# Kernel tuning notes

Measured on AMD Instinct MI355X. Metric: run time of the kernel, lower is better.

## Reference

```python
import jax, jax.numpy as jnp
import numpy as np

B, T, C = 8, 4096, 192
HIMG, WIMG = 64, 64
NH, HS = 24, 8
MIX_DIM, DECAY_DIM = 32, 64


def _conv2d(x, w, pad):
    # x: [B, C, H, W], w: [Cout, Cin, kh, kw]
    return jax.lax.conv_general_dilated(
        x, w, (1, 1), [(pad, pad), (pad, pad)],
        dimension_numbers=('NCHW', 'OIHW', 'NCHW'))


def setup_inputs() -> dict:
    key = jax.random.key(0)
    ks = jax.random.split(key, 26)
    f = jax.random.normal
    s = 1.0 / np.sqrt(C)
    return {
        'x': f(ks[0], (B, T, C), jnp.float32),
        'maa_x': f(ks[1], (1, 1, C), jnp.float32) * 0.1,
        'maa_w': f(ks[2], (1, 1, C), jnp.float32) * 0.1,
        'maa_k': f(ks[3], (1, 1, C), jnp.float32) * 0.1,
        'maa_v': f(ks[4], (1, 1, C), jnp.float32) * 0.1,
        'maa_r': f(ks[5], (1, 1, C), jnp.float32) * 0.1,
        'maa_g': f(ks[6], (1, 1, C), jnp.float32) * 0.1,
        'maa_w1': f(ks[7], (C, 5 * MIX_DIM), jnp.float32) * 0.01,
        'maa_w2': f(ks[8], (5, MIX_DIM, C), jnp.float32) * 0.01,
        'decay_w1': f(ks[9], (C, DECAY_DIM), jnp.float32) * 0.01,
        'decay_w2': f(ks[10], (DECAY_DIM, C), jnp.float32) * 0.01,
        'spatial_decay': f(ks[11], (1, 1, C), jnp.float32) * 0.5,
        'u': f(ks[12], (NH, HS), jnp.float32) * 0.5,
        'Wr': f(ks[13], (C, C), jnp.float32) * s,
        'Wk': f(ks[14], (C, C), jnp.float32) * s,
        'Wv': f(ks[15], (C, C), jnp.float32) * s,
        'Wg': f(ks[16], (C, C), jnp.float32) * s,
        'Wo': f(ks[17], (C, C), jnp.float32) * s,
        'ln_g': jnp.ones((C,), jnp.float32),
        'ln_b': jnp.zeros((C,), jnp.float32),
        'w_lp': f(ks[18], (C, C), jnp.float32) * s,
        'w_hd': f(ks[19], (C, C, 3), jnp.float32) * s,
        'w_vd': f(ks[20], (C, C, 3), jnp.float32) * s,
        'w_cd': f(ks[21], (C, C, 3, 3), jnp.float32) * (s / 3.0),
        'theta_cd': jnp.full((1,), 0.7, jnp.float32),
    }


def _diff_conv_mix(x2d, w_lp, w_hd, w_vd, w_cd, theta_cd):
    Cc = x2d.shape[1]
    # laplacian-pattern conv from a 1x1 weight (Conv2d_lp)
    k9 = jnp.zeros((Cc, Cc, 9), x2d.dtype)
    k9 = k9.at[:, :, jnp.array([1, 3, 5, 7])].set(w_lp[:, :, None])
    k9 = k9.at[:, :, 4].set(-4.0 * w_lp)
    out = _conv2d(x2d, k9.reshape(Cc, Cc, 3, 3), 1)
    # horizontal difference conv (Conv2d_hd)
    k9 = jnp.zeros((Cc, Cc, 9), x2d.dtype)
    k9 = k9.at[:, :, jnp.array([0, 3, 6])].set(w_hd)
    k9 = k9.at[:, :, jnp.array([2, 5, 8])].set(-w_hd)
    out = out + _conv2d(x2d, k9.reshape(Cc, Cc, 3, 3), 1)
    # vertical difference conv (Conv2d_vd)
    k9 = jnp.zeros((Cc, Cc, 9), x2d.dtype)
    k9 = k9.at[:, :, jnp.array([0, 1, 2])].set(w_vd)
    k9 = k9.at[:, :, jnp.array([6, 7, 8])].set(-w_vd)
    out = out + _conv2d(x2d, k9.reshape(Cc, Cc, 3, 3), 1)
    # central difference conv (Conv2d_cd): normal conv + 1x1 (-theta * kernel sum)
    out = out + _conv2d(x2d, w_cd, 1)
    kd = jnp.sum(w_cd, axis=(2, 3), keepdims=True) * (-theta_cd[0])
    out = out + _conv2d(x2d, kd, 0)
    return out


def reference(x, maa_x, maa_w, maa_k, maa_v, maa_r, maa_g, maa_w1, maa_w2,
              decay_w1, decay_w2, spatial_decay, u, Wr, Wk, Wv, Wg, Wo,
              ln_g, ln_b, w_lp, w_hd, w_vd, w_cd, theta_cd):
    Bb, Tt, Cc = x.shape
    x2d = x.transpose(0, 2, 1).reshape(Bb, Cc, HIMG, WIMG)
    shifted = _diff_conv_mix(x2d, w_lp, w_hd, w_vd, w_cd, theta_cd)
    xx = shifted.reshape(Bb, Cc, Tt).transpose(0, 2, 1) - x  # spatial shift delta

    # data-dependent token mixing (RWKV6 maa)
    xxx = x + xx * maa_x
    tmp = jnp.tanh(xxx @ maa_w1).reshape(Bb, Tt, 5, MIX_DIM)
    m = jnp.einsum('btfd,fdc->fbtc', tmp, maa_w2)  # [5, B, T, C]
    mw, mk, mv, mr, mg = m[0], m[1], m[2], m[3], m[4]
    xw = x + xx * (maa_w + mw)
    xk = x + xx * (maa_k + mk)
    xv = x + xx * (maa_v + mv)
    xr = x + xx * (maa_r + mr)
    xg = x + xx * (maa_g + mg)

    r = xr @ Wr
    k = xk @ Wk
    v = xv @ Wv
    g = jax.nn.silu(xg @ Wg)
    w = spatial_decay + jnp.tanh(xw @ decay_w1) @ decay_w2  # [B, T, C]

    # WKV6 linear recurrence, fp32 state, per-head [HS, HS]
    rh = r.reshape(Bb, Tt, NH, HS).astype(jnp.float32)
    kh = k.reshape(Bb, Tt, NH, HS).astype(jnp.float32)
    vh = v.reshape(Bb, Tt, NH, HS).astype(jnp.float32)
    dh = jnp.exp(-jnp.exp(w.astype(jnp.float32))).reshape(Bb, Tt, NH, HS)
    uf = u.astype(jnp.float32)

    def step(S, inp):  # S: [B, NH, HS(j key), HS(i value)]
        rt, kt, vt, dt = inp  # each [B, NH, HS]
        kv = kt[..., :, None] * vt[..., None, :]
        yt = jnp.einsum('bhj,bhji->bhi', rt, S + uf[None, :, :, None] * kv)
        return dt[..., None] * S + kv, yt

    xs = tuple(a.transpose(1, 0, 2, 3) for a in (rh, kh, vh, dh))  # time-major
    S0 = jnp.zeros((Bb, NH, HS, HS), jnp.float32)
    _, ys = jax.lax.scan(step, S0, xs)
    y = ys.transpose(1, 0, 2, 3).reshape(Bb, Tt, Cc).astype(x.dtype)

    # ln_x then gated output projection
    mu = jnp.mean(y, axis=-1, keepdims=True)
    var = jnp.mean((y - mu) ** 2, axis=-1, keepdims=True)
    yn = (y - mu) * jax.lax.rsqrt(var + 1e-5) * ln_g + ln_b
    return (yn * g) @ Wo
```

## Files before the change

kernel.cpp:

```cpp
#include <hip/hip_runtime.h>
#include <hip/hip_bf16.h>

#define Bq 8
#define Tq 4096
#define Cq 192
#define NHq 24
#define HSq 8
#define Mq (Bq * Tq)

#define CLq 64
#define NCHq (Tq / CLq)
#define TSq 32

typedef short short8 __attribute__((ext_vector_type(8)));
typedef float f32x4 __attribute__((ext_vector_type(4)));

__device__ __forceinline__ unsigned short f2bf(float f) {
    union { float f; unsigned u; } v; v.f = f;
    unsigned u = v.u;
    return (unsigned short)((u + 0x7FFFu + ((u >> 16) & 1u)) >> 16);
}

__global__ void prep_weights_kernel(const float* __restrict__ w_lp,
                                    const float* __restrict__ w_hd,
                                    const float* __restrict__ w_vd,
                                    const float* __restrict__ w_cd,
                                    const float* __restrict__ theta,
                                    unsigned short* __restrict__ Wg) {
    int idx = blockIdx.x * 256 + threadIdx.x;
    if (idx >= Cq * Cq) return;
    int cout = idx / Cq, cin = idx - cout * Cq;
    float t9[9];
#pragma unroll
    for (int t = 0; t < 9; ++t) t9[t] = 0.f;
    float lp = w_lp[idx];
    t9[1] += lp; t9[3] += lp; t9[5] += lp; t9[7] += lp; t9[4] -= 4.f * lp;
    float h0 = w_hd[idx * 3 + 0], h1 = w_hd[idx * 3 + 1], h2 = w_hd[idx * 3 + 2];
    t9[0] += h0; t9[3] += h1; t9[6] += h2;
    t9[2] -= h0; t9[5] -= h1; t9[8] -= h2;
    float v0 = w_vd[idx * 3 + 0], v1 = w_vd[idx * 3 + 1], v2 = w_vd[idx * 3 + 2];
    t9[0] += v0; t9[1] += v1; t9[2] += v2;
    t9[6] -= v0; t9[7] -= v1; t9[8] -= v2;
    float sum = 0.f;
#pragma unroll
    for (int t = 0; t < 9; ++t) {
        float cdv = w_cd[idx * 9 + t];
        t9[t] += cdv; sum += cdv;
    }
    t9[4] -= theta[0] * sum;
#pragma unroll
    for (int t = 0; t < 9; ++t)
        Wg[(size_t)cout * 1728 + t * Cq + cin] = f2bf(t9[t]);
}

__global__ void wtrans_kernel(const float* __restrict__ W,
                              unsigned short* __restrict__ Wt, int K, int N) {
    int idx = blockIdx.x * 256 + threadIdx.x;
    if (idx >= N * K) return;
    int n = idx / K, k = idx - n * K;
    Wt[idx] = f2bf(W[(size_t)k * N + n]);
}

__global__ void w2t_kernel(const float* __restrict__ w2,
                           unsigned short* __restrict__ w2t) {
    int idx = blockIdx.x * 256 + threadIdx.x;
    if (idx >= 5 * 192 * 32) return;
    int f = idx / (192 * 32), rem = idx - f * 192 * 32;
    int n = rem >> 5, k = rem & 31;
    w2t[idx] = f2bf(w2[(size_t)(f * 32 + k) * Cq + n]);
}

__global__ __launch_bounds__(256) void halo_kernel(
    const float* __restrict__ x, unsigned short* __restrict__ xh) {
    int idx = blockIdx.x * 256 + threadIdx.x;
    int c4 = (idx % 48) * 4;
    int cell = idx / 48;
    int hx = cell % 66;
    int rest = cell / 66;
    int hy = rest % 66;
    int bb = rest / 66;
    ushort4 o = make_ushort4(0, 0, 0, 0);
    if (hy >= 1 && hy <= 64 && hx >= 1 && hx <= 64) {
        size_t g = ((size_t)(bb << 12) + (hy - 1) * 64 + (hx - 1)) * Cq + c4;
        float4 v = *(const float4*)&x[g];
        o = make_ushort4(f2bf(v.x), f2bf(v.y), f2bf(v.z), f2bf(v.w));
    }
    *(ushort4*)&xh[(size_t)cell * Cq + c4] = o;
}

__global__ __launch_bounds__(256) void xxx_kernel(
    const float* __restrict__ x, const float* __restrict__ xx,
    const float* __restrict__ maa_x, unsigned short* __restrict__ out) {
    size_t g = ((size_t)blockIdx.x * 256 + threadIdx.x) * 4;
    int c = (int)(g % Cq);
    float4 xv = *(const float4*)&x[g];
    float4 dv = *(const float4*)&xx[g];
    float4 mv = *(const float4*)&maa_x[c];
    ushort4 o = make_ushort4(f2bf(fmaf(dv.x, mv.x, xv.x)), f2bf(fmaf(dv.y, mv.y, xv.y)),
                             f2bf(fmaf(dv.z, mv.z, xv.z)), f2bf(fmaf(dv.w, mv.w, xv.w)));
    *(ushort4*)&out[g] = o;
}

#define GBM 128
#define GBN 64
#define GBK 64

template <int ALOAD, int EPI, int OBF16>
__global__ __launch_bounds__(256) void mgemm_kernel(
    const unsigned short* __restrict__ Asrc,
    const unsigned short* __restrict__ Wt,
    void* __restrict__ Cv, int N, int K,
    const float* __restrict__ aux0) {
    __shared__ unsigned char lds[(GBM + GBN) * GBK * 2];
    unsigned char* Alds = lds;
    unsigned char* Blds = lds + GBM * GBK * 2;
    float* C = (float*)Cv;
    unsigned short* Cb = (unsigned short*)Cv;

    const int tid = threadIdx.x;
    const int wid = tid >> 6, lane = tid & 63;
    const int llo = lane & 15, lhi = lane >> 4;
    const int m0 = blockIdx.x * GBM, n0 = blockIdx.y * GBN;

    f32x4 acc[2][4];
#pragma unroll
    for (int a = 0; a < 2; ++a)
#pragma unroll
        for (int b = 0; b < 4; ++b) {
            f32x4 z = {0.f, 0.f, 0.f, 0.f};
            acc[a][b] = z;
        }

    for (int k0 = 0; k0 < K; k0 += GBK) {
        __syncthreads();
#pragma unroll
        for (int rep = 0; rep < 4; ++rep) {
            int c = tid + rep * 256;
            int row = c >> 3, kseg = c & 7;
            int m = m0 + row;
            short8 val;
            if (ALOAD == 3) {
                val = *(const short8*)&Asrc[(size_t)m * K + k0 + kseg * 8];
            } else {
                int tap = k0 / Cq;
                int cinb = k0 - tap * Cq;
                int t3 = tap / 3;
                int bb = m >> 12, pos = m & 4095;
                int hy = (pos >> 6) + t3;
                int hx = (pos & 63) + tap - t3 * 3;
                size_t g = ((size_t)bb * 4356 + hy * 66 + hx) * Cq + cinb + kseg * 8;
                val = *(const short8*)&Asrc[g];
            }
            *(short8*)(Alds + row * 128 + ((kseg * 16) ^ ((row & 7) << 4))) = val;
        }
#pragma unroll
        for (int rep = 0; rep < 2; ++rep) {
            int c = tid + rep * 256;
            int row = c >> 3, kseg = c & 7;
            int n = n0 + row;
            short8 val = {0, 0, 0, 0, 0, 0, 0, 0};
            if (n < N) val = *(const short8*)&Wt[(size_t)n * K + k0 + kseg * 8];
            *(short8*)(Blds + row * 128 + ((kseg * 16) ^ ((row & 7) << 4))) = val;
        }
        __syncthreads();
#pragma unroll
        for (int kc = 0; kc < 2; ++kc) {
            int kb = kc * 64 + lhi * 16;
            short8 af[2], bq[4];
#pragma unroll
            for (int mf = 0; mf < 2; ++mf) {
                int row = wid * 32 + mf * 16 + llo;
                af[mf] = *(const short8*)(Alds + row * 128 + (kb ^ ((row & 7) << 4)));
            }
#pragma unroll
            for (int nf = 0; nf < 4; ++nf) {
                int row = nf * 16 + llo;
                bq[nf] = *(const short8*)(Blds + row * 128 + (kb ^ ((row & 7) << 4)));
            }
#pragma unroll
            for (int mf = 0; mf < 2; ++mf)
#pragma unroll
                for (int nf = 0; nf < 4; ++nf)
                    acc[mf][nf] = __builtin_amdgcn_mfma_f32_16x16x32_bf16(
                        af[mf], bq[nf], acc[mf][nf], 0, 0, 0);
        }
    }
#pragma unroll
    for (int mf = 0; mf < 2; ++mf) {
#pragma unroll
        for (int nf = 0; nf < 4; ++nf) {
            int n = n0 + nf * 16 + llo;
            if (n >= N) continue;
#pragma unroll
            for (int r = 0; r < 4; ++r) {
                int m = m0 + wid * 32 + mf * 16 + lhi * 4 + r;
                float val = acc[mf][nf][r];
                if (EPI == 1) val -= aux0[(size_t)m * N + n];
                else if (EPI == 2) val = tanhf(val);
                else if (EPI == 3) val = val / (1.f + expf(-val));
                else if (EPI == 4) val = expf(-expf(aux0[n] + val));
                if (OBF16) Cb[(size_t)m * N + n] = f2bf(val);
                else C[(size_t)m * N + n] = val;
            }
        }
    }
}

__global__ __launch_bounds__(256) void mix5_kernel(
    const float* __restrict__ x, const float* __restrict__ xx,
    const unsigned short* __restrict__ tmp_bf,
    const unsigned short* __restrict__ w2t,
    const float* __restrict__ maa_w, const float* __restrict__ maa_k,
    const float* __restrict__ maa_v, const float* __restrict__ maa_r,
    const float* __restrict__ maa_g,
    unsigned short* __restrict__ xw, unsigned short* __restrict__ xr,
    unsigned short* __restrict__ xk, unsigned short* __restrict__ xv,
    unsigned short* __restrict__ xg) {
    const int tid = threadIdx.x;
    const int wid = tid >> 6, lane = tid & 63;
    const int llo = lane & 15, lhi = lane >> 4;
    const int mb = blockIdx.x * 128 + wid * 32;
    const int nb = blockIdx.y * 64;

    short8 aw[5][4];
#pragma unroll
    for (int f = 0; f < 5; ++f)
#pragma unroll
        for (int nf = 0; nf < 4; ++nf)
            aw[f][nf] = *(const short8*)&w2t[((size_t)f * Cq + nb + nf * 16 + llo) * 32 + lhi * 8];

#pragma unroll
    for (int sub = 0; sub < 2; ++sub) {
        short8 bt[5];
        {
            const unsigned short* trow = &tmp_bf[(size_t)(mb + sub * 16 + llo) * 160 + lhi * 8];
#pragma unroll
            for (int f = 0; f < 5; ++f) bt[f] = *(const short8*)&trow[f * 32];
        }
#pragma unroll
        for (int nf = 0; nf < 4; ++nf) {
            f32x4 acc[5];
#pragma unroll
            for (int f = 0; f < 5; ++f) {
                f32x4 z = {0.f, 0.f, 0.f, 0.f};
                acc[f] = __builtin_amdgcn_mfma_f32_16x16x32_bf16(aw[f][nf], bt[f], z, 0, 0, 0);
            }
            int m = mb + sub * 16 + llo;
            int n0 = nb + nf * 16 + lhi * 4;
            size_t g = (size_t)m * Cq + n0;
            float4 xv4 = *(const float4*)&x[g];
            float4 xx4 = *(const float4*)&xx[g];
            float4 mw4 = *(const float4*)&maa_w[n0];
            float4 mk4 = *(const float4*)&maa_k[n0];
            float4 mv4 = *(const float4*)&maa_v[n0];
            float4 mr4 = *(const float4*)&maa_r[n0];
            float4 mg4 = *(const float4*)&maa_g[n0];
            float xvv[4] = {xv4.x, xv4.y, xv4.z, xv4.w};
            float xxv[4] = {xx4.x, xx4.y, xx4.z, xx4.w};
            float mwv[4] = {mw4.x, mw4.y, mw4.z, mw4.w};
            float mkv[4] = {mk4.x, mk4.y, mk4.z, mk4.w};
            float mvv[4] = {mv4.x, mv4.y, mv4.z, mv4.w};
            float mrv[4] = {mr4.x, mr4.y, mr4.z, mr4.w};
            float mgv[4] = {mg4.x, mg4.y, mg4.z, mg4.w};
            ushort4 ow, ok, ov, orr, og;
            unsigned short* owp = (unsigned short*)&ow;
            unsigned short* okp = (unsigned short*)&ok;
            unsigned short* ovp = (unsigned short*)&ov;
            unsigned short* orp = (unsigned short*)&orr;
            unsigned short* ogp = (unsigned short*)&og;
#pragma unroll
            for (int r = 0; r < 4; ++r) {
                owp[r] = f2bf(fmaf(xxv[r], mwv[r] + acc[0][r], xvv[r]));
                okp[r] = f2bf(fmaf(xxv[r], mkv[r] + acc[1][r], xvv[r]));
                ovp[r] = f2bf(fmaf(xxv[r], mvv[r] + acc[2][r], xvv[r]));
                orp[r] = f2bf(fmaf(xxv[r], mrv[r] + acc[3][r], xvv[r]));
                ogp[r] = f2bf(fmaf(xxv[r], mgv[r] + acc[4][r], xvv[r]));
            }
            *(ushort4*)&xw[g] = ow;
            *(ushort4*)&xk[g] = ok;
            *(ushort4*)&xv[g] = ov;
            *(ushort4*)&xr[g] = orr;
            *(ushort4*)&xg[g] = og;
        }
    }
}

__global__ __launch_bounds__(64) void wkv_pass1_kernel(
    const float* __restrict__ k, const float* __restrict__ v,
    const float* __restrict__ d,
    float* __restrict__ Dbuf, float* __restrict__ Cbuf) {
    int chunk = blockIdx.x, hg = blockIdx.y, b = blockIdx.z;
    int lane = threadIdx.x;
    int slot = lane >> 3, i = lane & 7;
    int cbase = hg * 64;
    size_t gbase = ((size_t)b * Tq + (size_t)chunk * CLq) * Cq + cbase;
    __shared__ float ks[TSq][64], vs[TSq][64], ds[TSq][64];
    float S[8], D[8];
#pragma unroll
    for (int j = 0; j < 8; ++j) { S[j] = 0.f; D[j] = 1.f; }
    for (int t0 = 0; t0 < CLq; t0 += TSq) {
        int f = lane & 15, r4 = lane >> 4;
#pragma unroll
        for (int p = 0; p < 8; ++p) {
            int row = r4 + p * 4;
            size_t g = gbase + (size_t)(t0 + row) * Cq + f * 4;
            *(float4*)&ks[row][f * 4] = *(const float4*)&k[g];
            *(float4*)&vs[row][f * 4] = *(const float4*)&v[g];
            *(float4*)&ds[row][f * 4] = *(const float4*)&d[g];
        }
        __syncthreads();
#pragma unroll 8
        for (int t = 0; t < TSq; ++t) {
            float vv = vs[t][lane];
            float4 ka = *(const float4*)&ks[t][slot * 8];
            float4 kb = *(const float4*)&ks[t][slot * 8 + 4];
            float4 da = *(const float4*)&ds[t][slot * 8];
            float4 db = *(const float4*)&ds[t][slot * 8 + 4];
            float kk[8] = {ka.x, ka.y, ka.z, ka.w, kb.x, kb.y, kb.z, kb.w};
            float dd[8] = {da.x, da.y, da.z, da.w, db.x, db.y, db.z, db.w};
#pragma unroll
            for (int j = 0; j < 8; ++j) {
                float kv = kk[j] * vv;
                S[j] = fmaf(dd[j], S[j], kv);
                D[j] *= dd[j];
            }
        }
        __syncthreads();
    }
    size_t dbase = (((size_t)b * NCHq + chunk) * NHq + hg * 8) * 8;
    Dbuf[dbase + lane] = D[i];
    size_t cb = (((size_t)b * NCHq + chunk) * NHq + (hg * 8 + slot)) * 64 + i;
#pragma unroll
    for (int j = 0; j < 8; ++j) Cbuf[cb + j * 8] = S[j];
}

__global__ __launch_bounds__(64) void wkv_pass2_kernel(
    const float* __restrict__ Dbuf, const float* __restrict__ Cbuf,
    float* __restrict__ Sbuf) {
    int bh = blockIdx.x;
    int lane = threadIdx.x;
    int j = lane >> 3, i = lane & 7;
    int b = bh / NHq, h = bh - b * NHq;
    float S = 0.f;
    size_t stride = (size_t)NHq * 64;
    size_t base = ((size_t)b * NCHq * NHq + h) * 64 + j * 8 + i;
    size_t dstride = (size_t)NHq * 8;
    size_t dbase = ((size_t)b * NCHq * NHq + h) * 8 + j;
#pragma unroll 4
    for (int c = 0; c < NCHq; ++c) {
        Sbuf[base + c * stride] = S;
        float D = Dbuf[dbase + c * dstride];
        float C = Cbuf[base + c * stride];
        S = fmaf(D, S, C);
    }
}

__global__ __launch_bounds__(64) void wkv_pass3_kernel(
    const float* __restrict__ r, const float* __restrict__ k,
    const float* __restrict__ v, const float* __restrict__ d,
    const float* __restrict__ u, const float* __restrict__ Sbuf,
    float* __restrict__ y) {
    int chunk = blockIdx.x, hg = blockIdx.y, b = blockIdx.z;
    int lane = threadIdx.x;
    int slot = lane >> 3, i = lane & 7;
    int h = hg * 8 + slot;
    int cbase = hg * 64;
    size_t gbase = ((size_t)b * Tq + (size_t)chunk * CLq) * Cq + cbase;
    __shared__ float rs[TSq][64], ks[TSq][64], vs[TSq][64], ds[TSq][64];
    float S[8], uu[8];
    size_t sb = (((size_t)b * NCHq + chunk) * NHq + h) * 64 + i;
#pragma unroll
    for (int j = 0; j < 8; ++j) {
        S[j] = Sbuf[sb + j * 8];
        uu[j] = u[h * 8 + j];
    }
    for (int t0 = 0; t0 < CLq; t0 += TSq) {
        int f = lane & 15, r4 = lane >> 4;
#pragma unroll
        for (int p = 0; p < 8; ++p) {
            int row = r4 + p * 4;
            size_t g = gbase + (size_t)(t0 + row) * Cq + f * 4;
            *(float4*)&rs[row][f * 4] = *(const float4*)&r[g];
            *(float4*)&ks[row][f * 4] = *(const float4*)&k[g];
            *(float4*)&vs[row][f * 4] = *(const float4*)&v[g];
            *(float4*)&ds[row][f * 4] = *(const float4*)&d[g];
        }
        __syncthreads();
#pragma unroll 8
        for (int t = 0; t < TSq; ++t) {
            float vv = vs[t][lane];
            float4 ra = *(const float4*)&rs[t][slot * 8];
            float4 rb = *(const float4*)&rs[t][slot * 8 + 4];
            float4 ka = *(const float4*)&ks[t][slot * 8];
            float4 kb = *(const float4*)&ks[t][slot * 8 + 4];
            float4 da = *(const float4*)&ds[t][slot * 8];
            float4 db = *(const float4*)&ds[t][slot * 8 + 4];
            float rr[8] = {ra.x, ra.y, ra.z, ra.w, rb.x, rb.y, rb.z, rb.w};
            float kk[8] = {ka.x, ka.y, ka.z, ka.w, kb.x, kb.y, kb.z, kb.w};
            float dd[8] = {da.x, da.y, da.z, da.w, db.x, db.y, db.z, db.w};
            float yv = 0.f;
#pragma unroll
            for (int j = 0; j < 8; ++j) {
                float kv = kk[j] * vv;
                yv = fmaf(rr[j], fmaf(uu[j], kv, S[j]), yv);
                S[j] = fmaf(dd[j], S[j], kv);
            }
            y[gbase + (size_t)(t0 + t) * Cq + lane] = yv;
        }
        __syncthreads();
    }
}

__global__ __launch_bounds__(256) void ln_gate_kernel(
    const float* __restrict__ y, const float* __restrict__ g,
    const float* __restrict__ ln_g, const float* __restrict__ ln_b,
    unsigned short* __restrict__ out) {
    int row = blockIdx.x * 4 + (threadIdx.x >> 6);
    int lane = threadIdx.x & 63;
    const float* yr = y + (size_t)row * Cq;
    float a0 = yr[lane], a1 = yr[lane + 64], a2 = yr[lane + 128];
    float s = a0 + a1 + a2;
    float ss = a0 * a0 + a1 * a1 + a2 * a2;
#pragma unroll
    for (int m = 1; m < 64; m <<= 1) {
        s += __shfl_xor(s, m);
        ss += __shfl_xor(ss, m);
    }
    float mu = s * (1.f / 192.f);
    float var = ss * (1.f / 192.f) - mu * mu;
    float rstd = rsqrtf(var + 1e-5f);
    const float* gr = g + (size_t)row * Cq;
    unsigned short* orow = out + (size_t)row * Cq;
#pragma unroll
    for (int q = 0; q < 3; ++q) {
        int cc = lane + q * 64;
        float yn = (yr[cc] - mu) * rstd * ln_g[cc] + ln_b[cc];
        orow[cc] = f2bf(yn * gr[cc]);
    }
}

extern "C" void kernel_launch(void* const* d_in, const int* in_sizes, int n_in,
                              void* d_out, int out_size, void* d_ws, size_t ws_size,
                              hipStream_t stream) {
    const float* x        = (const float*)d_in[0];
    const float* maa_x    = (const float*)d_in[1];
    const float* maa_w    = (const float*)d_in[2];
    const float* maa_k    = (const float*)d_in[3];
    const float* maa_v    = (const float*)d_in[4];
    const float* maa_r    = (const float*)d_in[5];
    const float* maa_g    = (const float*)d_in[6];
    const float* maa_w1   = (const float*)d_in[7];
    const float* maa_w2   = (const float*)d_in[8];
    const float* decay_w1 = (const float*)d_in[9];
    const float* decay_w2 = (const float*)d_in[10];
    const float* sdecay   = (const float*)d_in[11];
    const float* u        = (const float*)d_in[12];
    const float* Wr       = (const float*)d_in[13];
    const float* Wk       = (const float*)d_in[14];
    const float* Wv       = (const float*)d_in[15];
    const float* Wgp      = (const float*)d_in[16];
    const float* Wo       = (const float*)d_in[17];
    const float* ln_g     = (const float*)d_in[18];
    const float* ln_b     = (const float*)d_in[19];
    const float* w_lp     = (const float*)d_in[20];
    const float* w_hd     = (const float*)d_in[21];
    const float* w_vd     = (const float*)d_in[22];
    const float* w_cd     = (const float*)d_in[23];
    const float* theta    = (const float*)d_in[24];
    float* out = (float*)d_out;

    const size_t BIG = (size_t)Mq * Cq;
    float* ws = (float*)d_ws;
    unsigned short* Wgt_conv = (unsigned short*)ws;
    unsigned short* Wt_maa = Wgt_conv + (size_t)Cq * 1728;
    unsigned short* Wt_r = Wt_maa + 160 * Cq;
    unsigned short* Wt_k = Wt_r + Cq * Cq;
    unsigned short* Wt_v = Wt_k + Cq * Cq;
    unsigned short* Wt_g = Wt_v + Cq * Cq;
    unsigned short* Wt_o = Wt_g + Cq * Cq;
    unsigned short* w2t  = Wt_o + Cq * Cq;
    unsigned short* Wt_d1 = w2t + 5 * 192 * 32;
    unsigned short* Wt_d2 = Wt_d1 + 64 * Cq;
    float* tmp  = ws + 331776;
    float* wtmp = tmp + (size_t)Mq * 160;
    float* buf0 = wtmp + (size_t)Mq * 64;
    float* buf1 = buf0 + BIG;
    float* buf2 = buf1 + BIG;
    float* buf3 = buf2 + BIG;
    float* buf4 = buf3 + BIG;
    float* buf5 = buf4 + BIG;

    unsigned short* tmp_bf = (unsigned short*)tmp;
    float* Dbuf = tmp + (size_t)Mq * 80;
    float* Cbuf = Dbuf + (size_t)Bq * NCHq * NHq * 8;
    float* Sbuf = Cbuf + (size_t)Bq * NCHq * NHq * 64;
    unsigned short* gate_b = (unsigned short*)(Sbuf + (size_t)Bq * NCHq * NHq * 64);

    unsigned short* x_halo = (unsigned short*)buf1;
    unsigned short* xw_b   = (unsigned short*)buf1;
    unsigned short* xxx_b  = (unsigned short*)(buf2 + BIG / 2);
    unsigned short* xv_b   = (unsigned short*)buf2;
    unsigned short* xg_b   = xxx_b;
    unsigned short* xr_b   = (unsigned short*)buf5;
    unsigned short* xk_b   = (unsigned short*)(buf5 + BIG / 2);
    unsigned short* wtmp_b = (unsigned short*)wtmp;

    dim3 blk(256);
    dim3 mg(Mq / GBM, 3);
    dim3 ew(Mq * Cq / 4 / 256);

    prep_weights_kernel<<<dim3(144), blk, 0, stream>>>(w_lp, w_hd, w_vd, w_cd, theta, Wgt_conv);
    wtrans_kernel<<<dim3(120), blk, 0, stream>>>(maa_w1, Wt_maa, Cq, 160);
    wtrans_kernel<<<dim3(144), blk, 0, stream>>>(Wr, Wt_r, Cq, Cq);
    wtrans_kernel<<<dim3(144), blk, 0, stream>>>(Wk, Wt_k, Cq, Cq);
    wtrans_kernel<<<dim3(144), blk, 0, stream>>>(Wv, Wt_v, Cq, Cq);
    wtrans_kernel<<<dim3(144), blk, 0, stream>>>(Wgp, Wt_g, Cq, Cq);
    wtrans_kernel<<<dim3(144), blk, 0, stream>>>(Wo, Wt_o, Cq, Cq);
    w2t_kernel<<<dim3(120), blk, 0, stream>>>(maa_w2, w2t);
    wtrans_kernel<<<dim3(48), blk, 0, stream>>>(decay_w1, Wt_d1, Cq, 64);
    wtrans_kernel<<<dim3(48), blk, 0, stream>>>(decay_w2, Wt_d2, 64, Cq);
    halo_kernel<<<dim3(8 * 66 * 66 * 48 / 256), blk, 0, stream>>>(x, x_halo);
    mgemm_kernel<1, 1, 0><<<mg, blk, 0, stream>>>(x_halo, Wgt_conv, buf0, Cq, 1728, x);
    xxx_kernel<<<ew, blk, 0, stream>>>(x, buf0, maa_x, xxx_b);
    mgemm_kernel<3, 2, 1><<<mg, blk, 0, stream>>>(xxx_b, Wt_maa, tmp_bf, 160, Cq, nullptr);
    mix5_kernel<<<dim3(Mq / 128, 3), blk, 0, stream>>>(
        x, buf0, tmp_bf, w2t, maa_w, maa_k, maa_v, maa_r, maa_g,
        xw_b, xr_b, xk_b, xv_b, xg_b);
    mgemm_kernel<3, 0, 0><<<mg, blk, 0, stream>>>(xv_b, Wt_v, buf3, Cq, Cq, nullptr);
    mgemm_kernel<3, 3, 0><<<mg, blk, 0, stream>>>(xg_b, Wt_g, buf4, Cq, Cq, nullptr);
    mgemm_kernel<3, 0, 0><<<mg, blk, 0, stream>>>(xr_b, Wt_r, buf0, Cq, Cq, nullptr);
    mgemm_kernel<3, 0, 0><<<mg, blk, 0, stream>>>(xk_b, Wt_k, buf2, Cq, Cq, nullptr);
    mgemm_kernel<3, 2, 1><<<dim3(Mq / GBM, 1), blk, 0, stream>>>(xw_b, Wt_d1, wtmp_b, 64, Cq, nullptr);
    mgemm_kernel<3, 4, 0><<<mg, blk, 0, stream>>>(wtmp_b, Wt_d2, buf5, Cq, 64, sdecay);
    wkv_pass1_kernel<<<dim3(NCHq, 3, Bq), dim3(64), 0, stream>>>(buf2, buf3, buf5, Dbuf, Cbuf);
    wkv_pass2_kernel<<<dim3(Bq * NHq), dim3(64), 0, stream>>>(Dbuf, Cbuf, Sbuf);
    wkv_pass3_kernel<<<dim3(NCHq, 3, Bq), dim3(64), 0, stream>>>(buf0, buf2, buf3, buf5, u, Sbuf, buf1);
    ln_gate_kernel<<<dim3(Mq / 4), blk, 0, stream>>>(buf1, buf4, ln_g, ln_b, gate_b);
    mgemm_kernel<3, 0, 0><<<mg, blk, 0, stream>>>(gate_b, Wt_o, out, Cq, Cq, nullptr);
}
```

Before: 388.4 us.

## Fuse xxx into conv GEMM epilogue and store intermediates as bf16

Folds the x-minus-conv difference and the maa_x mix into the conv GEMM epilogue, which removes the separate xxx kernel and one fp32 round trip. It also switches r/k/v/g projections, the wkv output y and the xx tensor to bf16 storage, and mix5 reads x from the bf16 halo buffer, to cut memory traffic across the pipeline. mix5 blocks shrink to 128 threads. In exchange, more intermediates are rounded to bf16, and x itself is taken from a bf16 copy in several places, which lowers accuracy.

```diff
diff --git a/kernel.cpp b/kernel.cpp
--- a/kernel.cpp
+++ b/kernel.cpp
@@ -19,6 +19,13 @@
     union { float f; unsigned u; } v; v.f = f;
     unsigned u = v.u;
     return (unsigned short)((u + 0x7FFFu + ((u >> 16) & 1u)) >> 16);
+}
+__device__ __forceinline__ float bf2f(unsigned short u) {
+    union { unsigned u; float f; } v; v.u = (unsigned)u << 16;
+    return v.f;
+}
+__device__ __forceinline__ float4 bf4_to_f4(ushort4 u) {
+    return make_float4(bf2f(u.x), bf2f(u.y), bf2f(u.z), bf2f(u.w));
 }
 
 __global__ void prep_weights_kernel(const float* __restrict__ w_lp,
@@ -88,19 +95,6 @@
     *(ushort4*)&xh[(size_t)cell * Cq + c4] = o;
 }
 
-__global__ __launch_bounds__(256) void xxx_kernel(
-    const float* __restrict__ x, const float* __restrict__ xx,
-    const float* __restrict__ maa_x, unsigned short* __restrict__ out) {
-    size_t g = ((size_t)blockIdx.x * 256 + threadIdx.x) * 4;
-    int c = (int)(g % Cq);
-    float4 xv = *(const float4*)&x[g];
-    float4 dv = *(const float4*)&xx[g];
-    float4 mv = *(const float4*)&maa_x[c];
-    ushort4 o = make_ushort4(f2bf(fmaf(dv.x, mv.x, xv.x)), f2bf(fmaf(dv.y, mv.y, xv.y)),
-                             f2bf(fmaf(dv.z, mv.z, xv.z)), f2bf(fmaf(dv.w, mv.w, xv.w)));
-    *(ushort4*)&out[g] = o;
-}
-
 #define GBM 128
 #define GBN 64
 #define GBK 64
@@ -110,7 +104,9 @@
     const unsigned short* __restrict__ Asrc,
     const unsigned short* __restrict__ Wt,
     void* __restrict__ Cv, int N, int K,
-    const float* __restrict__ aux0) {
+    const float* __restrict__ aux0,
+    const unsigned short* __restrict__ xh,
+    unsigned short* __restrict__ C2) {
     __shared__ unsigned char lds[(GBM + GBN) * GBK * 2];
     unsigned char* Alds = lds;
     unsigned char* Blds = lds + GBM * GBK * 2;
@@ -185,6 +181,25 @@
                         af[mf], bq[nf], acc[mf][nf], 0, 0, 0);
         }
     }
+    if (EPI == 5) {
+#pragma unroll
+        for (int mf = 0; mf < 2; ++mf)
+#pragma unroll
+            for (int nf = 0; nf < 4; ++nf) {
+                int n = n0 + nf * 16 + llo;
+#pragma unroll
+                for (int r = 0; r < 4; ++r) {
+                    int m = m0 + wid * 32 + mf * 16 + lhi * 4 + r;
+                    int pos = m & 4095, bb = m >> 12;
+                    size_t cell = (size_t)bb * 4356 + ((pos >> 6) + 1) * 66 + (pos & 63) + 1;
+                    float xv = bf2f(xh[cell * Cq + n]);
+                    float xxv = acc[mf][nf][r] - xv;
+                    Cb[(size_t)m * Cq + n] = f2bf(xxv);
+                    C2[(size_t)m * Cq + n] = f2bf(fmaf(xxv, aux0[n], xv));
+                }
+            }
+        return;
+    }
 #pragma unroll
     for (int mf = 0; mf < 2; ++mf) {
 #pragma unroll
@@ -195,8 +210,7 @@
             for (int r = 0; r < 4; ++r) {
                 int m = m0 + wid * 32 + mf * 16 + lhi * 4 + r;
                 float val = acc[mf][nf][r];
-                if (EPI == 1) val -= aux0[(size_t)m * N + n];
-                else if (EPI == 2) val = tanhf(val);
+                if (EPI == 2) val = tanhf(val);
                 else if (EPI == 3) val = val / (1.f + expf(-val));
                 else if (EPI == 4) val = expf(-expf(aux0[n] + val));
                 if (OBF16) Cb[(size_t)m * N + n] = f2bf(val);
@@ -206,8 +220,9 @@
     }
 }
 
-__global__ __launch_bounds__(256) void mix5_kernel(
-    const float* __restrict__ x, const float* __restrict__ xx,
+__global__ __launch_bounds__(128) void mix5_kernel(
+    const unsigned short* __restrict__ xh,
+    const unsigned short* __restrict__ xxb,
     const unsigned short* __restrict__ tmp_bf,
     const unsigned short* __restrict__ w2t,
     const float* __restrict__ maa_w, const float* __restrict__ maa_k,
@@ -219,7 +234,7 @@
     const int tid = threadIdx.x;
     const int wid = tid >> 6, lane = tid & 63;
     const int llo = lane & 15, lhi = lane >> 4;
-    const int mb = blockIdx.x * 128 + wid * 32;
+    const int mb = blockIdx.x * 64 + wid * 32;
     const int nb = blockIdx.y * 64;
 
     short8 aw[5][4];
@@ -237,6 +252,9 @@
 #pragma unroll
             for (int f = 0; f < 5; ++f) bt[f] = *(const short8*)&trow[f * 32];
         }
+        int m = mb + sub * 16 + llo;
+        int pos = m & 4095, bb = m >> 12;
+        size_t xbase = ((size_t)bb * 4356 + ((pos >> 6) + 1) * 66 + (pos & 63) + 1) * Cq;
 #pragma unroll
         for (int nf = 0; nf < 4; ++nf) {
             f32x4 acc[5];
@@ -245,11 +263,10 @@
                 f32x4 z = {0.f, 0.f, 0.f, 0.f};
                 acc[f] = __builtin_amdgcn_mfma_f32_16x16x32_bf16(aw[f][nf], bt[f], z, 0, 0, 0);
             }
-            int m = mb + sub * 16 + llo;
             int n0 = nb + nf * 16 + lhi * 4;
             size_t g = (size_t)m * Cq + n0;
-            float4 xv4 = *(const float4*)&x[g];
-            float4 xx4 = *(const float4*)&xx[g];
+            float4 xv4 = bf4_to_f4(*(const ushort4*)&xh[xbase + n0]);
+            float4 xx4 = bf4_to_f4(*(const ushort4*)&xxb[g]);
             float4 mw4 = *(const float4*)&maa_w[n0];
             float4 mk4 = *(const float4*)&maa_k[n0];
             float4 mv4 = *(const float4*)&maa_v[n0];
@@ -286,7 +303,7 @@
 }
 
 __global__ __launch_bounds__(64) void wkv_pass1_kernel(
-    const float* __restrict__ k, const float* __restrict__ v,
+    const unsigned short* __restrict__ k, const unsigned short* __restrict__ v,
     const float* __restrict__ d,
     float* __restrict__ Dbuf, float* __restrict__ Cbuf) {
     int chunk = blockIdx.x, hg = blockIdx.y, b = blockIdx.z;
@@ -304,8 +321,8 @@
         for (int p = 0; p < 8; ++p) {
             int row = r4 + p * 4;
             size_t g = gbase + (size_t)(t0 + row) * Cq + f * 4;
-            *(float4*)&ks[row][f * 4] = *(const float4*)&k[g];
-            *(float4*)&vs[row][f * 4] = *(const float4*)&v[g];
+            *(float4*)&ks[row][f * 4] = bf4_to_f4(*(const ushort4*)&k[g]);
+            *(float4*)&vs[row][f * 4] = bf4_to_f4(*(const ushort4*)&v[g]);
             *(float4*)&ds[row][f * 4] = *(const float4*)&d[g];
         }
         __syncthreads();
@@ -356,10 +373,10 @@
 }
 
 __global__ __launch_bounds__(64) void wkv_pass3_kernel(
-    const float* __restrict__ r, const float* __restrict__ k,
-    const float* __restrict__ v, const float* __restrict__ d,
+    const unsigned short* __restrict__ r, const unsigned short* __restrict__ k,
+    const unsigned short* __restrict__ v, const float* __restrict__ d,
     const float* __restrict__ u, const float* __restrict__ Sbuf,
-    float* __restrict__ y) {
+    unsigned short* __restrict__ y) {
     int chunk = blockIdx.x, hg = blockIdx.y, b = blockIdx.z;
     int lane = threadIdx.x;
     int slot = lane >> 3, i = lane & 7;
@@ -380,9 +397,9 @@
         for (int p = 0; p < 8; ++p) {
             int row = r4 + p * 4;
             size_t g = gbase + (size_t)(t0 + row) * Cq + f * 4;
-            *(float4*)&rs[row][f * 4] = *(const float4*)&r[g];
-            *(float4*)&ks[row][f * 4] = *(const float4*)&k[g];
-            *(float4*)&vs[row][f * 4] = *(const float4*)&v[g];
+            *(float4*)&rs[row][f * 4] = bf4_to_f4(*(const ushort4*)&r[g]);
+            *(float4*)&ks[row][f * 4] = bf4_to_f4(*(const ushort4*)&k[g]);
+            *(float4*)&vs[row][f * 4] = bf4_to_f4(*(const ushort4*)&v[g]);
             *(float4*)&ds[row][f * 4] = *(const float4*)&d[g];
         }
         __syncthreads();
@@ -405,20 +422,20 @@
                 yv = fmaf(rr[j], fmaf(uu[j], kv, S[j]), yv);
                 S[j] = fmaf(dd[j], S[j], kv);
             }
-            y[gbase + (size_t)(t0 + t) * Cq + lane] = yv;
+            y[gbase + (size_t)(t0 + t) * Cq + lane] = f2bf(yv);
         }
         __syncthreads();
     }
 }
 
 __global__ __launch_bounds__(256) void ln_gate_kernel(
-    const float* __restrict__ y, const float* __restrict__ g,
+    const unsigned short* __restrict__ y, const unsigned short* __restrict__ g,
     const float* __restrict__ ln_g, const float* __restrict__ ln_b,
     unsigned short* __restrict__ out) {
     int row = blockIdx.x * 4 + (threadIdx.x >> 6);
     int lane = threadIdx.x & 63;
-    const float* yr = y + (size_t)row * Cq;
-    float a0 = yr[lane], a1 = yr[lane + 64], a2 = yr[lane + 128];
+    const unsigned short* yr = y + (size_t)row * Cq;
+    float a0 = bf2f(yr[lane]), a1 = bf2f(yr[lane + 64]), a2 = bf2f(yr[lane + 128]);
     float s = a0 + a1 + a2;
     float ss = a0 * a0 + a1 * a1 + a2 * a2;
 #pragma unroll
@@ -429,13 +446,14 @@
     float mu = s * (1.f / 192.f);
     float var = ss * (1.f / 192.f) - mu * mu;
     float rstd = rsqrtf(var + 1e-5f);
-    const float* gr = g + (size_t)row * Cq;
+    const unsigned short* gr = g + (size_t)row * Cq;
     unsigned short* orow = out + (size_t)row * Cq;
+    float aa[3] = {a0, a1, a2};
 #pragma unroll
     for (int q = 0; q < 3; ++q) {
         int cc = lane + q * 64;
-        float yn = (yr[cc] - mu) * rstd * ln_g[cc] + ln_b[cc];
-        orow[cc] = f2bf(yn * gr[cc]);
+        float yn = (aa[q] - mu) * rstd * ln_g[cc] + ln_b[cc];
+        orow[cc] = f2bf(yn * bf2f(gr[cc]));
     }
 }
 
@@ -494,20 +512,28 @@
     float* Dbuf = tmp + (size_t)Mq * 80;
     float* Cbuf = Dbuf + (size_t)Bq * NCHq * NHq * 8;
     float* Sbuf = Cbuf + (size_t)Bq * NCHq * NHq * 64;
-    unsigned short* gate_b = (unsigned short*)(Sbuf + (size_t)Bq * NCHq * NHq * 64);
 
     unsigned short* x_halo = (unsigned short*)buf1;
-    unsigned short* xw_b   = (unsigned short*)buf1;
+    unsigned short* y_b    = (unsigned short*)buf1;
+    unsigned short* xx_b   = (unsigned short*)buf0;
+    unsigned short* xw_b   = (unsigned short*)(buf0 + BIG / 2);
+    unsigned short* r_b    = (unsigned short*)buf0;
     unsigned short* xxx_b  = (unsigned short*)(buf2 + BIG / 2);
+    unsigned short* xg_b   = xxx_b;
     unsigned short* xv_b   = (unsigned short*)buf2;
-    unsigned short* xg_b   = xxx_b;
+    unsigned short* k_b    = (unsigned short*)buf2;
+    unsigned short* gate_b = (unsigned short*)buf2;
+    unsigned short* v_b    = (unsigned short*)buf3;
+    unsigned short* g_b    = (unsigned short*)buf4;
     unsigned short* xr_b   = (unsigned short*)buf5;
     unsigned short* xk_b   = (unsigned short*)(buf5 + BIG / 2);
+    float* d_f             = buf5;
     unsigned short* wtmp_b = (unsigned short*)wtmp;
 
     dim3 blk(256);
     dim3 mg(Mq / GBM, 3);
-    dim3 ew(Mq * Cq / 4 / 256);
+    const unsigned short* nosrc = nullptr;
+    unsigned short* nodst = nullptr;
 
     prep_weights_kernel<<<dim3(144), blk, 0, stream>>>(w_lp, w_hd, w_vd, w_cd, theta, Wgt_conv);
     wtrans_kernel<<<dim3(120), blk, 0, stream>>>(maa_w1, Wt_maa, Cq, 160);
@@ -520,21 +546,20 @@
     wtrans_kernel<<<dim3(48), blk, 0, stream>>>(decay_w1, Wt_d1, Cq, 64);
     wtrans_kernel<<<dim3(48), blk, 0, stream>>>(decay_w2, Wt_d2, 64, Cq);
     halo_kernel<<<dim3(8 * 66 * 66 * 48 / 256), blk, 0, stream>>>(x, x_halo);
-    mgemm_kernel<1, 1, 0><<<mg, blk, 0, stream>>>(x_halo, Wgt_conv, buf0, Cq, 1728, x);
-    xxx_kernel<<<ew, blk, 0, stream>>>(x, buf0, maa_x, xxx_b);
-    mgemm_kernel<3, 2, 1><<<mg, blk, 0, stream>>>(xxx_b, Wt_maa, tmp_bf, 160, Cq, nullptr);
-    mix5_kernel<<<dim3(Mq / 128, 3), blk, 0, stream>>>(
-        x, buf0, tmp_bf, w2t, maa_w, maa_k, maa_v, maa_r, maa_g,
+    mgemm_kernel<1, 5, 1><<<mg, blk, 0, stream>>>(x_halo, Wgt_conv, xx_b, Cq, 1728, maa_x, x_halo, xxx_b);
+    mgemm_kernel<3, 2, 1><<<mg, blk, 0, stream>>>(xxx_b, Wt_maa, tmp_bf, 160, Cq, nullptr, nosrc, nodst);
+    mix5_kernel<<<dim3(Mq / 64, 3), dim3(128), 0, stream>>>(
+        x_halo, xx_b, tmp_bf, w2t, maa_w, maa_k, maa_v, maa_r, maa_g,
         xw_b, xr_b, xk_b, xv_b, xg_b);
-    mgemm_kernel<3, 0, 0><<<mg, blk, 0, stream>>>(xv_b, Wt_v, buf3, Cq, Cq, nullptr);
-    mgemm_kernel<3, 3, 0><<<mg, blk, 0, stream>>>(xg_b, Wt_g, buf4, Cq, Cq, nullptr);
-    mgemm_kernel<3, 0, 0><<<mg, blk, 0, stream>>>(xr_b, Wt_r, buf0, Cq, Cq, nullptr);
-    mgemm_kernel<3, 0, 0><<<mg, blk, 0, stream>>>(xk_b, Wt_k, buf2, Cq, Cq, nullptr);
-    mgemm_kernel<3, 2, 1><<<dim3(Mq / GBM, 1), blk, 0, stream>>>(xw_b, Wt_d1, wtmp_b, 64, Cq, nullptr);
-    mgemm_kernel<3, 4, 0><<<mg, blk, 0, stream>>>(wtmp_b, Wt_d2, buf5, Cq, 64, sdecay);
-    wkv_pass1_kernel<<<dim3(NCHq, 3, Bq), dim3(64), 0, stream>>>(buf2, buf3, buf5, Dbuf, Cbuf);
+    mgemm_kernel<3, 0, 1><<<mg, blk, 0, stream>>>(xv_b, Wt_v, v_b, Cq, Cq, nullptr, nosrc, nodst);
+    mgemm_kernel<3, 3, 1><<<mg, blk, 0, stream>>>(xg_b, Wt_g, g_b, Cq, Cq, nullptr, nosrc, nodst);
+    mgemm_kernel<3, 0, 1><<<mg, blk, 0, stream>>>(xr_b, Wt_r, r_b, Cq, Cq, nullptr, nosrc, nodst);
+    mgemm_kernel<3, 0, 1><<<mg, blk, 0, stream>>>(xk_b, Wt_k, k_b, Cq, Cq, nullptr, nosrc, nodst);
+    mgemm_kernel<3, 2, 1><<<dim3(Mq / GBM, 1), blk, 0, stream>>>(xw_b, Wt_d1, wtmp_b, 64, Cq, nullptr, nosrc, nodst);
+    mgemm_kernel<3, 4, 0><<<mg, blk, 0, stream>>>(wtmp_b, Wt_d2, d_f, Cq, 64, sdecay, nosrc, nodst);
+    wkv_pass1_kernel<<<dim3(NCHq, 3, Bq), dim3(64), 0, stream>>>(k_b, v_b, d_f, Dbuf, Cbuf);
     wkv_pass2_kernel<<<dim3(Bq * NHq), dim3(64), 0, stream>>>(Dbuf, Cbuf, Sbuf);
-    wkv_pass3_kernel<<<dim3(NCHq, 3, Bq), dim3(64), 0, stream>>>(buf0, buf2, buf3, buf5, u, Sbuf, buf1);
-    ln_gate_kernel<<<dim3(Mq / 4), blk, 0, stream>>>(buf1, buf4, ln_g, ln_b, gate_b);
-    mgemm_kernel<3, 0, 0><<<mg, blk, 0, stream>>>(gate_b, Wt_o, out, Cq, Cq, nullptr);
-}
+    wkv_pass3_kernel<<<dim3(NCHq, 3, Bq), dim3(64), 0, stream>>>(r_b, k_b, v_b, d_f, u, Sbuf, y_b);
+    ln_gate_kernel<<<dim3(Mq / 4), blk, 0, stream>>>(y_b, g_b, ln_g, ln_b, gate_b);
+    mgemm_kernel<3, 0, 0><<<mg, blk, 0, stream>>>(gate_b, Wt_o, out, Cq, Cq, nullptr, nosrc, nodst);
+}
```

Result: faster. 359.7 us (-7.4%).
